# Performance work log

Measured on AMD Instinct MI355X. Metric: run time of the kernel, lower is better.

Reference implementation:

```python
import jax, jax.numpy as jnp
import numpy as np

B, G, D, H, W = 2, 8, 32, 128, 160
NEIGH = 9           # evaluate_neighbors
PROP = 1            # propagation_out_range - 1
PAD1 = int(np.sqrt(NEIGH) / 2) + PROP      # = 2
PAD2 = PAD1 * 2                            # = 4


def setup_inputs() -> dict:
    key = jax.random.key(0)
    ks = jax.random.split(key, 8)
    x1 = jax.random.normal(ks[0], (B, G, D, H, W), jnp.float32)
    offset = jax.random.uniform(ks[1], (B, 2 * NEIGH, H, W), jnp.float32)
    weight = jax.random.uniform(ks[2], (B, 1, H, W), jnp.float32)
    # 1x1x1 Conv3d weights stored as [out_ch, in_ch]; BN folded to scale/bias (eval mode)
    w0 = jax.random.normal(ks[3], (16, G), jnp.float32) * 0.1
    bn0_scale = jnp.ones((16,), jnp.float32)
    bn0_bias = jnp.zeros((16,), jnp.float32)
    w1 = jax.random.normal(ks[4], (8, 16), jnp.float32) * 0.1
    bn1_scale = jnp.ones((8,), jnp.float32)
    bn1_bias = jnp.zeros((8,), jnp.float32)
    w_sim = jax.random.normal(ks[5], (1, 8), jnp.float32) * 0.1
    b_sim = jnp.zeros((1,), jnp.float32)
    return {"x1": x1, "offset": offset, "weight": weight,
            "w0": w0, "bn0_scale": bn0_scale, "bn0_bias": bn0_bias,
            "w1": w1, "bn1_scale": bn1_scale, "bn1_bias": bn1_bias,
            "w_sim": w_sim, "b_sim": b_sim}


def _conv1x1_bn_relu(x, w, scale, bias):
    # x: [B,Cin,D,H,W], w: [Cout,Cin]
    y = jnp.einsum('bcdhw,oc->bodhw', x, w)
    return jax.nn.relu(y * scale[None, :, None, None, None] + bias[None, :, None, None, None])


def reference(x1, offset, weight, w0, bn0_scale, bn0_bias, w1, bn1_scale, bn1_bias, w_sim, b_sim):
    h = _conv1x1_bn_relu(x1, w0, bn0_scale, bn0_bias)          # [B,16,D,H,W]
    h = _conv1x1_bn_relu(h, w1, bn1_scale, bn1_bias)            # [B,8,D,H,W]
    sim = jnp.einsum('bcdhw,oc->bodhw', h, w_sim) + b_sim[None, :, None, None, None]
    sim = sim[:, 0]                                             # [B,D,H,W]
    b, d, hgt, wid = sim.shape
    p1 = jnp.pad(sim, ((0, 0), (0, 0), (PAD1, PAD1), (PAD1, PAD1)), mode='reflect')
    p2 = jnp.pad(sim, ((0, 0), (0, 0), (PAD2, PAD2), (PAD2, PAD2)), mode='reflect')
    side = int(np.sqrt(NEIGH))  # 3
    acc = jnp.zeros_like(sim)
    for s in range(NEIGH):
        iy, ix = s // side, s % side
        # wide-dilation crop (stride (PROP+1)*2 = 4) over the double-padded map
        c2 = p2[:, :, iy * 4: iy * 4 + hgt, ix * 4: ix * 4 + wid]
        # narrow-dilation crop (stride PROP+1 = 2) over the single-padded map
        c1 = p1[:, :, iy * 2: iy * 2 + hgt, ix * 2: ix * 2 + wid]
        w_wide = offset[:, s][:, None]            # [B,1,H,W] -> broadcast over depth
        w_narrow = offset[:, s + NEIGH][:, None]
        acc = acc + (w_narrow * c1 + w_wide * c2) * 0.5
    return acc * weight                                          # weight [B,1,H,W]
```

## Files before the change

### kernel.cpp

```cpp
#include <hip/hip_runtime.h>

#define Bc 2
#define Gc 8
#define Dc 32
#define Hc 128
#define Wc 160
#define DHW (Dc * Hc * Wc)
#define HW (Hc * Wc)

__global__ __launch_bounds__(256) void mlp_kernel(
    const float* __restrict__ x1,
    const float* __restrict__ w0, const float* __restrict__ s0, const float* __restrict__ b0,
    const float* __restrict__ w1, const float* __restrict__ s1, const float* __restrict__ b1,
    const float* __restrict__ wsim, const float* __restrict__ bsim,
    float* __restrict__ sim)
{
    __shared__ float sm[289];
    const int tid = threadIdx.x;
    for (int i = tid; i < 289; i += 256) {
        float v;
        if (i < 128)      v = w0[i] * s0[i >> 3];
        else if (i < 144) v = b0[i - 128];
        else if (i < 272) v = w1[i - 144] * s1[(i - 144) >> 4];
        else if (i < 280) v = b1[i - 272];
        else if (i < 288) v = wsim[i - 280];
        else              v = bsim[0];
        sm[i] = v;
    }
    __syncthreads();
    const float* sw0 = sm;
    const float* sb0 = sm + 128;
    const float* sw1 = sm + 144;
    const float* sb1 = sm + 272;
    const float* sws = sm + 280;
    const float  sbs = sm[288];

    const int t   = blockIdx.x * 256 + tid;
    const int p   = t << 2;
    const int b   = p / DHW;
    const int dhw = p - b * DHW;
    const float* xb = x1 + (size_t)b * (Gc * DHW) + dhw;

    float4 xv[Gc];
#pragma unroll
    for (int g = 0; g < Gc; ++g)
        xv[g] = *reinterpret_cast<const float4*>(xb + g * DHW);

    float4 h0[16];
#pragma unroll
    for (int o = 0; o < 16; ++o) {
        float ax = sb0[o], ay = ax, az = ax, aw = ax;
#pragma unroll
        for (int g = 0; g < Gc; ++g) {
            const float wv = sw0[o * Gc + g];
            ax = fmaf(wv, xv[g].x, ax);
            ay = fmaf(wv, xv[g].y, ay);
            az = fmaf(wv, xv[g].z, az);
            aw = fmaf(wv, xv[g].w, aw);
        }
        h0[o].x = fmaxf(ax, 0.f);
        h0[o].y = fmaxf(ay, 0.f);
        h0[o].z = fmaxf(az, 0.f);
        h0[o].w = fmaxf(aw, 0.f);
    }

    float sx = sbs, sy = sbs, sz = sbs, sw = sbs;
#pragma unroll
    for (int c = 0; c < 8; ++c) {
        float ax = sb1[c], ay = ax, az = ax, aw = ax;
#pragma unroll
        for (int o = 0; o < 16; ++o) {
            const float wv = sw1[c * 16 + o];
            ax = fmaf(wv, h0[o].x, ax);
            ay = fmaf(wv, h0[o].y, ay);
            az = fmaf(wv, h0[o].z, az);
            aw = fmaf(wv, h0[o].w, aw);
        }
        const float ws = sws[c];
        sx = fmaf(ws, fmaxf(ax, 0.f), sx);
        sy = fmaf(ws, fmaxf(ay, 0.f), sy);
        sz = fmaf(ws, fmaxf(az, 0.f), sz);
        sw = fmaf(ws, fmaxf(aw, 0.f), sw);
    }

    float4 r; r.x = sx; r.y = sy; r.z = sz; r.w = sw;
    *reinterpret_cast<float4*>(sim + p) = r;
}

__global__ __launch_bounds__(256) void agg_kernel(
    const float* __restrict__ sim, const float* __restrict__ offset,
    const float* __restrict__ weight, float* __restrict__ out)
{
    const int l = blockIdx.x * 256 + threadIdx.x;
    const int w = l % Wc;
    int r = l / Wc;
    const int h = r % Hc;
    r /= Hc;
    const int dg = r & 3;
    const int b  = r >> 2;

    float off[18];
#pragma unroll
    for (int s = 0; s < 18; ++s)
        off[s] = offset[((b * 18 + s) * Hc + h) * Wc + w];
    const float wt = weight[b * HW + h * Wc + w];

    int idx1[9], idx2[9];
#pragma unroll
    for (int iy = 0; iy < 3; ++iy) {
        int y1 = h + (iy - 1) * 2; y1 = y1 < 0 ? -y1 : (y1 >= Hc ? 2 * Hc - 2 - y1 : y1);
        int y2 = h + (iy - 1) * 4; y2 = y2 < 0 ? -y2 : (y2 >= Hc ? 2 * Hc - 2 - y2 : y2);
#pragma unroll
        for (int ix = 0; ix < 3; ++ix) {
            int x1c = w + (ix - 1) * 2; x1c = x1c < 0 ? -x1c : (x1c >= Wc ? 2 * Wc - 2 - x1c : x1c);
            int x2c = w + (ix - 1) * 4; x2c = x2c < 0 ? -x2c : (x2c >= Wc ? 2 * Wc - 2 - x2c : x2c);
            idx1[iy * 3 + ix] = y1 * Wc + x1c;
            idx2[iy * 3 + ix] = y2 * Wc + x2c;
        }
    }

    const size_t base = (size_t)(b * Dc + dg * 8) * HW;
    const float* sp0 = sim + base;
    float* op0 = out + base + h * Wc + w;
#pragma unroll
    for (int d = 0; d < 8; ++d) {
        const float* sp = sp0 + d * HW;
        float a = 0.f;
#pragma unroll
        for (int s = 0; s < 9; ++s)
            a = fmaf(off[s + 9], sp[idx1[s]], fmaf(off[s], sp[idx2[s]], a));
        op0[d * HW] = a * 0.5f * wt;
    }
}

extern "C" void kernel_launch(void* const* d_in, const int* in_sizes, int n_in,
                              void* d_out, int out_size, void* d_ws, size_t ws_size,
                              hipStream_t stream)
{
    const float* x1     = (const float*)d_in[0];
    const float* offset = (const float*)d_in[1];
    const float* weight = (const float*)d_in[2];
    const float* w0     = (const float*)d_in[3];
    const float* s0     = (const float*)d_in[4];
    const float* b0     = (const float*)d_in[5];
    const float* w1     = (const float*)d_in[6];
    const float* s1     = (const float*)d_in[7];
    const float* b1     = (const float*)d_in[8];
    const float* wsim   = (const float*)d_in[9];
    const float* bsim   = (const float*)d_in[10];
    float* out = (float*)d_out;
    float* sim = (float*)d_ws;

    mlp_kernel<<<1280, 256, 0, stream>>>(x1, w0, s0, b0, w1, s1, b1, wsim, bsim, sim);
    agg_kernel<<<640, 256, 0, stream>>>(sim, offset, weight, out);
}
```

Before: 125.2 us.

## Fuse MLP and neighbor aggregation into one tiled kernel with shared-memory halo

Merges the per-voxel MLP and the 9-neighbor aggregation into a single kernel. Each block owns a 32x40 spatial tile at one depth slice, computes sim for the tile plus a 4-pixel reflected halo into shared memory, then aggregates from shared memory. This removes the global round trip of the sim intermediate and one launch. In exchange the halo pixels are recomputed (about 1.6x MLP work), offsets are now reloaded once per depth slice instead of once per 8 depths, and the halo edge loads are unaligned scalar reads.

```diff
diff --git a/kernel.cpp b/kernel.cpp
--- a/kernel.cpp
+++ b/kernel.cpp
@@ -5,18 +5,30 @@
 #define Dc 32
 #define Hc 128
 #define Wc 160
-#define DHW (Dc * Hc * Wc)
 #define HW (Hc * Wc)
+#define DHW (Dc * HW)
 
-__global__ __launch_bounds__(256) void mlp_kernel(
-    const float* __restrict__ x1,
+#define TH 32
+#define TW 40
+#define R  4
+#define SH (TH + 2 * R)
+#define SW (TW + 2 * R)
+#define SIMN (SH * SW)
+#define NQ (SIMN / 4)
+#define QPR (SW / 4)
+
+__global__ __launch_bounds__(256) void fused_kernel(
+    const float* __restrict__ x1, const float* __restrict__ offset,
+    const float* __restrict__ weight,
     const float* __restrict__ w0, const float* __restrict__ s0, const float* __restrict__ b0,
     const float* __restrict__ w1, const float* __restrict__ s1, const float* __restrict__ b1,
     const float* __restrict__ wsim, const float* __restrict__ bsim,
-    float* __restrict__ sim)
+    float* __restrict__ out)
 {
-    __shared__ float sm[289];
+    __shared__ __align__(16) float sms[SIMN];
+    __shared__ float smw[289];
     const int tid = threadIdx.x;
+
     for (int i = tid; i < 289; i += 256) {
         float v;
         if (i < 128)      v = w0[i] * s0[i >> 3];
@@ -25,111 +37,126 @@
         else if (i < 280) v = b1[i - 272];
         else if (i < 288) v = wsim[i - 280];
         else              v = bsim[0];
-        sm[i] = v;
-    }
-    __syncthreads();
-    const float* sw0 = sm;
-    const float* sb0 = sm + 128;
-    const float* sw1 = sm + 144;
-    const float* sb1 = sm + 272;
-    const float* sws = sm + 280;
-    const float  sbs = sm[288];
-
-    const int t   = blockIdx.x * 256 + tid;
-    const int p   = t << 2;
-    const int b   = p / DHW;
-    const int dhw = p - b * DHW;
-    const float* xb = x1 + (size_t)b * (Gc * DHW) + dhw;
-
-    float4 xv[Gc];
-#pragma unroll
-    for (int g = 0; g < Gc; ++g)
-        xv[g] = *reinterpret_cast<const float4*>(xb + g * DHW);
-
-    float4 h0[16];
-#pragma unroll
-    for (int o = 0; o < 16; ++o) {
-        float ax = sb0[o], ay = ax, az = ax, aw = ax;
-#pragma unroll
-        for (int g = 0; g < Gc; ++g) {
-            const float wv = sw0[o * Gc + g];
-            ax = fmaf(wv, xv[g].x, ax);
-            ay = fmaf(wv, xv[g].y, ay);
-            az = fmaf(wv, xv[g].z, az);
-            aw = fmaf(wv, xv[g].w, aw);
-        }
-        h0[o].x = fmaxf(ax, 0.f);
-        h0[o].y = fmaxf(ay, 0.f);
-        h0[o].z = fmaxf(az, 0.f);
-        h0[o].w = fmaxf(aw, 0.f);
+        smw[i] = v;
     }
 
-    float sx = sbs, sy = sbs, sz = sbs, sw = sbs;
+    const int blk = blockIdx.x;
+    const int d   = blk & 31;
+    const int t   = (blk >> 5) & 15;
+    const int b   = blk >> 9;
+    const int h0t = (t >> 2) * TH;
+    const int w0t = (t & 3) * TW;
+
+    __syncthreads();
+
+    const float* sw0 = smw;
+    const float* sb0 = smw + 128;
+    const float* sw1 = smw + 144;
+    const float* sb1 = smw + 272;
+    const float* sws = smw + 280;
+    const float  sbs = smw[288];
+
+    const float* xb = x1 + (size_t)b * (Gc * DHW) + (size_t)d * HW;
+
+    for (int q = tid; q < NQ; q += 256) {
+        const int ty  = q / QPR;
+        const int tx0 = (q - ty * QPR) * 4;
+        int gh = h0t - R + ty;
+        gh = gh < 0 ? -gh : (gh >= Hc ? 2 * Hc - 2 - gh : gh);
+        const int gw0 = w0t - R + tx0;
+
+        float4 xv[Gc];
+        if (gw0 >= 0 && gw0 <= Wc - 4) {
+            const float* p = xb + gh * Wc + gw0;
 #pragma unroll
-    for (int c = 0; c < 8; ++c) {
-        float ax = sb1[c], ay = ax, az = ax, aw = ax;
+            for (int g = 0; g < Gc; ++g)
+                xv[g] = *reinterpret_cast<const float4*>(p + g * DHW);
+        } else {
+            int gw[4];
+#pragma unroll
+            for (int j = 0; j < 4; ++j) {
+                int x = gw0 + j;
+                gw[j] = x < 0 ? -x : (x >= Wc ? 2 * Wc - 2 - x : x);
+            }
+            const float* p = xb + gh * Wc;
+#pragma unroll
+            for (int g = 0; g < Gc; ++g) {
+                xv[g].x = p[g * DHW + gw[0]];
+                xv[g].y = p[g * DHW + gw[1]];
+                xv[g].z = p[g * DHW + gw[2]];
+                xv[g].w = p[g * DHW + gw[3]];
+            }
+        }
+
+        float4 h0[16];
 #pragma unroll
         for (int o = 0; o < 16; ++o) {
-            const float wv = sw1[c * 16 + o];
-            ax = fmaf(wv, h0[o].x, ax);
-            ay = fmaf(wv, h0[o].y, ay);
-            az = fmaf(wv, h0[o].z, az);
-            aw = fmaf(wv, h0[o].w, aw);
+            float ax = sb0[o], ay = ax, az = ax, aw = ax;
+#pragma unroll
+            for (int g = 0; g < Gc; ++g) {
+                const float wv = sw0[o * Gc + g];
+                ax = fmaf(wv, xv[g].x, ax);
+                ay = fmaf(wv, xv[g].y, ay);
+                az = fmaf(wv, xv[g].z, az);
+                aw = fmaf(wv, xv[g].w, aw);
+            }
+            h0[o].x = fmaxf(ax, 0.f);
+            h0[o].y = fmaxf(ay, 0.f);
+            h0[o].z = fmaxf(az, 0.f);
+            h0[o].w = fmaxf(aw, 0.f);
         }
-        const float ws = sws[c];
-        sx = fmaf(ws, fmaxf(ax, 0.f), sx);
-        sy = fmaf(ws, fmaxf(ay, 0.f), sy);
-        sz = fmaf(ws, fmaxf(az, 0.f), sz);
-        sw = fmaf(ws, fmaxf(aw, 0.f), sw);
+
+        float sx = sbs, sy = sbs, sz = sbs, sw = sbs;
+#pragma unroll
+        for (int c = 0; c < 8; ++c) {
+            float ax = sb1[c], ay = ax, az = ax, aw = ax;
+#pragma unroll
+            for (int o = 0; o < 16; ++o) {
+                const float wv = sw1[c * 16 + o];
+                ax = fmaf(wv, h0[o].x, ax);
+                ay = fmaf(wv, h0[o].y, ay);
+                az = fmaf(wv, h0[o].z, az);
+                aw = fmaf(wv, h0[o].w, aw);
+            }
+            const float ws = sws[c];
+            sx = fmaf(ws, fmaxf(ax, 0.f), sx);
+            sy = fmaf(ws, fmaxf(ay, 0.f), sy);
+            sz = fmaf(ws, fmaxf(az, 0.f), sz);
+            sw = fmaf(ws, fmaxf(aw, 0.f), sw);
+        }
+
+        float4 r; r.x = sx; r.y = sy; r.z = sz; r.w = sw;
+        *reinterpret_cast<float4*>(&sms[q * 4]) = r;
     }
 
-    float4 r; r.x = sx; r.y = sy; r.z = sz; r.w = sw;
-    *reinterpret_cast<float4*>(sim + p) = r;
-}
+    __syncthreads();
 
-__global__ __launch_bounds__(256) void agg_kernel(
-    const float* __restrict__ sim, const float* __restrict__ offset,
-    const float* __restrict__ weight, float* __restrict__ out)
-{
-    const int l = blockIdx.x * 256 + threadIdx.x;
-    const int w = l % Wc;
-    int r = l / Wc;
-    const int h = r % Hc;
-    r /= Hc;
-    const int dg = r & 3;
-    const int b  = r >> 2;
+    const float* offb = offset + (size_t)b * 18 * HW;
+    const float* wtb  = weight + (size_t)b * HW;
+    float* outb = out + (size_t)(b * Dc + d) * HW;
 
-    float off[18];
 #pragma unroll
-    for (int s = 0; s < 18; ++s)
-        off[s] = offset[((b * 18 + s) * Hc + h) * Wc + w];
-    const float wt = weight[b * HW + h * Wc + w];
+    for (int k = 0; k < 5; ++k) {
+        const int idx = k * 256 + tid;
+        const int oy  = idx / TW;
+        const int ox  = idx - oy * TW;
+        const int hw  = (h0t + oy) * Wc + (w0t + ox);
 
-    int idx1[9], idx2[9];
+        float off[18];
 #pragma unroll
-    for (int iy = 0; iy < 3; ++iy) {
-        int y1 = h + (iy - 1) * 2; y1 = y1 < 0 ? -y1 : (y1 >= Hc ? 2 * Hc - 2 - y1 : y1);
-        int y2 = h + (iy - 1) * 4; y2 = y2 < 0 ? -y2 : (y2 >= Hc ? 2 * Hc - 2 - y2 : y2);
-#pragma unroll
-        for (int ix = 0; ix < 3; ++ix) {
-            int x1c = w + (ix - 1) * 2; x1c = x1c < 0 ? -x1c : (x1c >= Wc ? 2 * Wc - 2 - x1c : x1c);
-            int x2c = w + (ix - 1) * 4; x2c = x2c < 0 ? -x2c : (x2c >= Wc ? 2 * Wc - 2 - x2c : x2c);
-            idx1[iy * 3 + ix] = y1 * Wc + x1c;
-            idx2[iy * 3 + ix] = y2 * Wc + x2c;
-        }
-    }
+        for (int s = 0; s < 18; ++s)
+            off[s] = offb[s * HW + hw];
+        const float wt = wtb[hw] * 0.5f;
 
-    const size_t base = (size_t)(b * Dc + dg * 8) * HW;
-    const float* sp0 = sim + base;
-    float* op0 = out + base + h * Wc + w;
-#pragma unroll
-    for (int d = 0; d < 8; ++d) {
-        const float* sp = sp0 + d * HW;
+        const float* sp = sms + (oy + R) * SW + (ox + R);
         float a = 0.f;
 #pragma unroll
-        for (int s = 0; s < 9; ++s)
-            a = fmaf(off[s + 9], sp[idx1[s]], fmaf(off[s], sp[idx2[s]], a));
-        op0[d * HW] = a * 0.5f * wt;
+        for (int s = 0; s < 9; ++s) {
+            const int dy = s / 3 - 1, dx = s % 3 - 1;
+            a = fmaf(off[s + 9], sp[(dy * 2) * SW + dx * 2],
+                fmaf(off[s],     sp[(dy * 4) * SW + dx * 4], a));
+        }
+        outb[hw] = a * wt;
     }
 }
 
@@ -149,8 +176,8 @@
     const float* wsim   = (const float*)d_in[9];
     const float* bsim   = (const float*)d_in[10];
     float* out = (float*)d_out;
-    float* sim = (float*)d_ws;
 
-    mlp_kernel<<<1280, 256, 0, stream>>>(x1, w0, s0, b0, w1, s1, b1, wsim, bsim, sim);
-    agg_kernel<<<640, 256, 0, stream>>>(sim, offset, weight, out);
+    fused_kernel<<<1024, 256, 0, stream>>>(x1, offset, weight,
+                                           w0, s0, b0, w1, s1, b1, wsim, bsim,
+                                           out);
 }
```

Result: slower. 238.8 us (+90.7%).
